# Kernel tuning notes

Measured on AMD Instinct MI355X. Metric: run time of the kernel, lower is better.

Reference implementation:

```python
import jax, jax.numpy as jnp
import numpy as np

D_MODEL = 4096
N_EXPERTS = 64
LN_EPS = 1e-5


def setup_inputs() -> dict:
    key = jax.random.key(0)
    k_x, k_w, k_b = jax.random.split(key, 3)
    x = jax.random.normal(k_x, (4, 4096, D_MODEL), dtype=jnp.float32)
    # LayerNorm affine params (torch defaults: ones / zeros)
    gamma = jnp.ones((D_MODEL,), dtype=jnp.float32)
    beta = jnp.zeros((D_MODEL,), dtype=jnp.float32)
    # Linear(d_model, n): weight (n, d), bias (n) — kaiming-uniform-ish init
    bound = 1.0 / np.sqrt(D_MODEL)
    W = jax.random.uniform(k_w, (N_EXPERTS, D_MODEL), dtype=jnp.float32, minval=-bound, maxval=bound)
    b = jax.random.uniform(k_b, (N_EXPERTS,), dtype=jnp.float32, minval=-bound, maxval=bound)
    return {"x": x, "gamma": gamma, "beta": beta, "W": W, "b": b, "top_k": 2}


def reference(x, gamma, beta, W, b, top_k):
    # LayerNorm over last dim
    mu = jnp.mean(x, axis=-1, keepdims=True)
    var = jnp.mean(jnp.square(x - mu), axis=-1, keepdims=True)
    xn = (x - mu) * jax.lax.rsqrt(var + LN_EPS) * gamma + beta
    # Gate projection: (B,T,d) @ (d,n) -> (B,T,n)
    logits = jnp.einsum('btd,nd->btn', xn, W) + b
    weights = jax.nn.softmax(logits, axis=-1)  # (B,T,n)
    k = min(int(top_k), weights.shape[-1])
    topk_vals, indices = jax.lax.top_k(weights, k)  # (B,T,k)
    # scatter top-k values back to dense (B,T,n), then renormalize
    onehot = jax.nn.one_hot(indices, weights.shape[-1], dtype=weights.dtype)  # (B,T,k,n)
    sparse_w = jnp.einsum('btkn,btk->btn', onehot, topk_vals)
    sparse_w = sparse_w / (jnp.sum(sparse_w, axis=-1, keepdims=True) + 1e-8)
    # load-balance (entropy) loss on dense weights
    mean_w = jnp.mean(weights, axis=(0, 1))  # (n,)
    lb_loss = -jnp.sum(mean_w * jnp.log(mean_w + 1e-8))
    return sparse_w, indices, lb_loss
```

## Files before the change

kernel.cpp:

```cpp
#include <hip/hip_runtime.h>
#include <math.h>

#define D_MODEL 4096
#define N_EXP   64
#define N_ROWS  16384
#define LN_EPS  1e-5f
#define TMB     64
#define NBLK    (N_ROWS / TMB)

typedef __attribute__((ext_vector_type(4))) float f32x4;
typedef __attribute__((ext_vector_type(8))) short s16x8;

struct U4 { unsigned v[4]; };

__device__ __forceinline__ unsigned pkt(float a, float b) {
  unsigned ua = __builtin_bit_cast(unsigned, a);
  unsigned ub = __builtin_bit_cast(unsigned, b);
  return (ua >> 16) | (ub & 0xffff0000u);
}
__device__ __forceinline__ float lo2f(unsigned p) { return __builtin_bit_cast(float, p << 16); }
__device__ __forceinline__ float hi2f(unsigned p) { return __builtin_bit_cast(float, p & 0xffff0000u); }

__device__ __forceinline__ void split8(const float* f, U4& u1, U4& u2, U4& u3) {
#pragma unroll
  for (int i = 0; i < 4; ++i) {
    const float a = f[2 * i], b = f[2 * i + 1];
    const unsigned p1 = pkt(a, b);
    const float ra = a - lo2f(p1), rb = b - hi2f(p1);
    const unsigned p2 = pkt(ra, rb);
    const float sa = ra - lo2f(p2), sb = rb - hi2f(p2);
    u1.v[i] = p1; u2.v[i] = p2; u3.v[i] = pkt(sa, sb);
  }
}


__global__ __launch_bounds__(64) void prep_bpre(
    const float* __restrict__ W, const float* __restrict__ gamma,
    float* __restrict__ Bpre)
{
  const int b = blockIdx.x;
  const int kb32 = b >> 2, j0 = b & 3;
  const int L = threadIdx.x, q = L >> 4, c = L & 15;
  const int n  = j0 * 16 + c;
  const int k0 = kb32 * 32 + q * 8;
  const float4 w0 = *(const float4*)(W + (size_t)n * D_MODEL + k0);
  const float4 w1 = *(const float4*)(W + (size_t)n * D_MODEL + k0 + 4);
  const float4 g0 = *(const float4*)(gamma + k0);
  const float4 g1 = *(const float4*)(gamma + k0 + 4);
  float f[8] = {w0.x * g0.x, w0.y * g0.y, w0.z * g0.z, w0.w * g0.w,
                w1.x * g1.x, w1.y * g1.y, w1.z * g1.z, w1.w * g1.w};
  U4 u1, u2, u3;
  split8(f, u1, u2, u3);
  const size_t base = ((size_t)kb32 * 12 + j0 * 3) * 64 + L;
  *(float4*)(Bpre + (base + 0 * 64) * 4) = __builtin_bit_cast(float4, u1);
  *(float4*)(Bpre + (base + 1 * 64) * 4) = __builtin_bit_cast(float4, u2);
  *(float4*)(Bpre + (base + 2 * 64) * 4) = __builtin_bit_cast(float4, u3);
}

__global__ __launch_bounds__(256) void prep_gc(
    const float* __restrict__ W, const float* __restrict__ gamma,
    const float* __restrict__ beta, const float* __restrict__ bias,
    float* __restrict__ G, float* __restrict__ C)
{
  const int e = blockIdx.x, t = threadIdx.x;
  float sg = 0.f, sb = 0.f;
#pragma unroll
  for (int i = 0; i < 4; ++i) {
    const int d = (i * 256 + t) * 4;
    const float4 wv = *(const float4*)(W + (size_t)e * D_MODEL + d);
    const float4 gv = *(const float4*)(gamma + d);
    const float4 bv = *(const float4*)(beta + d);
    sg += wv.x * gv.x + wv.y * gv.y + wv.z * gv.z + wv.w * gv.w;
    sb += wv.x * bv.x + wv.y * bv.y + wv.z * bv.z + wv.w * bv.w;
  }
#pragma unroll
  for (int o = 32; o > 0; o >>= 1) {
    sg += __shfl_xor(sg, o, 64);
    sb += __shfl_xor(sb, o, 64);
  }
  __shared__ float rg_[4], rb_[4];
  const int wid = t >> 6, ln = t & 63;
  if (ln == 0) { rg_[wid] = sg; rb_[wid] = sb; }
  __syncthreads();
  if (t == 0) {
    G[e] = rg_[0] + rg_[1] + rg_[2] + rg_[3];
    C[e] = rb_[0] + rb_[1] + rb_[2] + rb_[3] + bias[e];
  }
}

__device__ __forceinline__ void loadA64(const float* aptr, int K0, float4 A[4]) {
  const float* ap = aptr + K0;
#pragma unroll
  for (int s = 0; s < 2; ++s) {
    A[2 * s]     = *(const float4*)(ap + s * 32);
    A[2 * s + 1] = *(const float4*)(ap + s * 32 + 4);
  }
}

__device__ __forceinline__ void gload_lds16(const float* g, const float4* l) {
  __builtin_amdgcn_global_load_lds(
      (const __attribute__((address_space(1))) void*)(g),
      (__attribute__((address_space(3))) void*)(l),
      16, 0, 0);
}

__device__ __forceinline__ void stage_chunk64(const float* __restrict__ Bpre,
                                              float4* dstbase, int kb32g, int g, int L)
{
  const float* src = Bpre + (((size_t)kb32g * 12 + g * 6) * 64 + L) * 4;
  float4* dst = dstbase + (size_t)(g * 6) * 64;
#pragma unroll
  for (int i = 0; i < 6; ++i)
    gload_lds16(src + (size_t)i * 256, dst + (size_t)i * 64);
}

__device__ __forceinline__ void compute_chunk64(
    const float4* __restrict__ buf, int L,
    const float4 A[4], f32x4 acc[4], float& Sp, float& Qp)
{
  const int PA[6] = {0, 0, 1, 0, 1, 2};
  const int PB[6] = {0, 1, 0, 2, 1, 0};
#pragma unroll
  for (int s = 0; s < 2; ++s) {
    s16x8 bf[4][3];
#pragma unroll
    for (int j0 = 0; j0 < 4; ++j0)
#pragma unroll
      for (int tt = 0; tt < 3; ++tt)
        bf[j0][tt] = __builtin_bit_cast(s16x8, buf[(size_t)(s * 12 + j0 * 3 + tt) * 64 + L]);
    const float4 a0 = A[2 * s], a1 = A[2 * s + 1];
    const float f[8] = {a0.x, a0.y, a0.z, a0.w, a1.x, a1.y, a1.z, a1.w};
#pragma unroll
    for (int i = 0; i < 8; ++i) { Sp += f[i]; Qp = fmaf(f[i], f[i], Qp); }
    U4 u1, u2, u3;
    split8(f, u1, u2, u3);
    const s16x8 af[3] = {__builtin_bit_cast(s16x8, u1),
                         __builtin_bit_cast(s16x8, u2),
                         __builtin_bit_cast(s16x8, u3)};
#pragma unroll
    for (int p = 0; p < 6; ++p)
#pragma unroll
      for (int j0 = 0; j0 < 4; ++j0)
        acc[j0] = __builtin_amdgcn_mfma_f32_16x16x32_bf16(af[PA[p]], bf[j0][PB[p]],
                                                          acc[j0], 0, 0, 0);
  }
}

__global__ __launch_bounds__(512, 2) void router_main(
    const float* __restrict__ x, const float* __restrict__ Bpre,
    const float* __restrict__ G, const float* __restrict__ C,
    float* __restrict__ out_sw, float* __restrict__ out_idx,
    float* __restrict__ out_partials, int k)
{
  const int t = threadIdx.x, w = t >> 6, L = t & 63;
  const int q = L >> 4, c = L & 15;
  const int g = w & 3;
  const int ks = w >> 2;
  const int blk = blockIdx.x;
  const int row0 = blk * TMB + g * 16;
  const int Kbase = ks * 2048;
  const int kb32base = ks * 64;

  const float* aptr = x + (size_t)(row0 + c) * D_MODEL + q * 8;

  union Smem {
    float4 B[2][2][24 * 64];
    struct { float red[4][64][19]; float sm[4][64]; } ep;
  };
  __shared__ Smem S;

  f32x4 acc[4];
#pragma unroll
  for (int j0 = 0; j0 < 4; ++j0) acc[j0] = (f32x4){0.f, 0.f, 0.f, 0.f};
  float Sp = 0.f, Qp = 0.f;

  float4 A0[4], A1[4];
  loadA64(aptr, Kbase, A0);
  stage_chunk64(Bpre, S.B[ks][0], kb32base, g, L);
  __syncthreads();

  for (int kb = 0; kb < 32; kb += 2) {
    stage_chunk64(Bpre, S.B[ks][1], kb32base + (kb + 1) * 2, g, L);
    loadA64(aptr, Kbase + (kb + 1) * 64, A1);
    compute_chunk64(S.B[ks][0], L, A0, acc, Sp, Qp);
    __syncthreads();

    if (kb + 2 < 32) stage_chunk64(Bpre, S.B[ks][0], kb32base + (kb + 2) * 2, g, L);
    loadA64(aptr, Kbase + ((kb + 2) & 31) * 64, A0);
    compute_chunk64(S.B[ks][1], L, A1, acc, Sp, Qp);
    __syncthreads();
  }

#pragma unroll
  for (int o = 16; o <= 32; o <<= 1) {
    Sp += __shfl_xor(Sp, o, 64);
    Qp += __shfl_xor(Qp, o, 64);
  }

  if (ks == 1) {
    float* dst = &S.ep.red[g][L][0];
#pragma unroll
    for (int j0 = 0; j0 < 4; ++j0)
#pragma unroll
      for (int i = 0; i < 4; ++i) dst[j0 * 4 + i] = acc[j0][i];
    dst[16] = Sp; dst[17] = Qp;
  }
  __syncthreads();

  if (ks == 0) {
    const float* sp_ = &S.ep.red[g][L][0];
#pragma unroll
    for (int j0 = 0; j0 < 4; ++j0)
#pragma unroll
      for (int i = 0; i < 4; ++i) acc[j0][i] += sp_[j0 * 4 + i];
    Sp += sp_[16]; Qp += sp_[17];

    const float mu = Sp * (1.f / D_MODEL);
    const float rs = rsqrtf(Qp * (1.f / D_MODEL) - mu * mu + LN_EPS);

    float Gv[4], Cv[4];
#pragma unroll
    for (int j0 = 0; j0 < 4; ++j0) { Gv[j0] = G[16 * j0 + c]; Cv[j0] = C[16 * j0 + c]; }

    float mw[4] = {0.f, 0.f, 0.f, 0.f};
#pragma unroll
    for (int i = 0; i < 4; ++i) {
      const int rloc = 4 * q + i;
      const int row  = row0 + rloc;
      const float mui = __shfl(mu, rloc, 64);
      const float rsi = __shfl(rs, rloc, 64);
      float l[4];
#pragma unroll
      for (int j0 = 0; j0 < 4; ++j0)
        l[j0] = rsi * (acc[j0][i] - mui * Gv[j0]) + Cv[j0];
      float mx = fmaxf(fmaxf(l[0], l[1]), fmaxf(l[2], l[3]));
#pragma unroll
      for (int o = 1; o < 16; o <<= 1) mx = fmaxf(mx, __shfl_xor(mx, o, 64));
      float p[4], ss = 0.f;
#pragma unroll
      for (int j0 = 0; j0 < 4; ++j0) { p[j0] = __expf(l[j0] - mx); ss += p[j0]; }
#pragma unroll
      for (int o = 1; o < 16; o <<= 1) ss += __shfl_xor(ss, o, 64);
      float wv[4];
#pragma unroll
      for (int j0 = 0; j0 < 4; ++j0) { wv[j0] = p[j0] / ss; mw[j0] += wv[j0]; }

      int ch[4];
      float denom = 0.f;
      for (int kk = 0; kk < k && kk < 4; ++kk) {
        float vb = -1.f; int eb = 1 << 30;
#pragma unroll
        for (int j0 = 0; j0 < 4; ++j0) {
          const int e = 16 * j0 + c;
          bool skip = false;
          for (int z = 0; z < kk; ++z) skip |= (ch[z] == e);
          const float cand = skip ? -1.f : wv[j0];
          if (cand > vb || (cand == vb && e < eb)) { vb = cand; eb = e; }
        }
#pragma unroll
        for (int o = 1; o < 16; o <<= 1) {
          const float ov = __shfl_xor(vb, o, 64);
          const int   oe = __shfl_xor(eb, o, 64);
          if (ov > vb || (ov == vb && oe < eb)) { vb = ov; eb = oe; }
        }
        ch[kk] = eb; denom += vb;
        if (c == 0) out_idx[(size_t)row * k + kk] = (float)eb;
      }
      denom += 1e-8f;
#pragma unroll
      for (int j0 = 0; j0 < 4; ++j0) {
        const int e = 16 * j0 + c;
        bool sel = false;
        for (int z = 0; z < k && z < 4; ++z) sel |= (ch[z] == e);
        out_sw[(size_t)row * N_EXP + e] = sel ? wv[j0] / denom : 0.f;
      }
    }

#pragma unroll
    for (int j0 = 0; j0 < 4; ++j0)
#pragma unroll
      for (int o = 16; o <= 32; o <<= 1) mw[j0] += __shfl_xor(mw[j0], o, 64);
    if (q == 0) {
#pragma unroll
      for (int j0 = 0; j0 < 4; ++j0) S.ep.sm[g][16 * j0 + c] = mw[j0];
    }
  }
  __syncthreads();
  if (t < 64)
    out_partials[blk * 64 + t] = S.ep.sm[0][t] + S.ep.sm[1][t] + S.ep.sm[2][t] + S.ep.sm[3][t];
}

__global__ __launch_bounds__(256) void loss_kernel(
    const float* __restrict__ partials, float* __restrict__ out_loss)
{
  const int t = threadIdx.x, e = t & 63, qq = t >> 6;
  float s = 0.f;
#pragma unroll 8
  for (int b = 0; b < 64; ++b) s += partials[(qq * 64 + b) * 64 + e];
  __shared__ float sh[256];
  sh[t] = s;
  __syncthreads();
  if (t < 64) {
    const float m = (sh[t] + sh[64 + t] + sh[128 + t] + sh[192 + t]) * (1.f / N_ROWS);
    float v = -m * logf(m + 1e-8f);
#pragma unroll
    for (int o = 32; o > 0; o >>= 1) v += __shfl_xor(v, o, 64);
    if (t == 0) out_loss[0] = v;
  }
}

extern "C" void kernel_launch(void* const* d_in, const int* in_sizes, int n_in,
                              void* d_out, int out_size, void* d_ws, size_t ws_size,
                              hipStream_t stream)
{
  const float* x     = (const float*)d_in[0];
  const float* gamma = (const float*)d_in[1];
  const float* beta  = (const float*)d_in[2];
  const float* W     = (const float*)d_in[3];
  const float* bias  = (const float*)d_in[4];

  float* ws       = (float*)d_ws;
  float* Bpre     = ws;
  float* G        = ws + 393216;
  float* C        = ws + 393280;
  float* partials = ws + 393344;

  int k = (out_size - N_ROWS * N_EXP - 1) / N_ROWS;
  if (k < 1) k = 1;
  if (k > 4) k = 4;

  float* out      = (float*)d_out;
  float* out_sw   = out;
  float* out_idx  = out + (size_t)N_ROWS * N_EXP;
  float* out_loss = out + (size_t)N_ROWS * N_EXP + (size_t)N_ROWS * k;

  hipLaunchKernelGGL(prep_bpre, dim3(512), dim3(64), 0, stream, W, gamma, Bpre);
  hipLaunchKernelGGL(prep_gc, dim3(N_EXP), dim3(256), 0, stream, W, gamma, beta, bias, G, C);
  hipLaunchKernelGGL(router_main, dim3(NBLK), dim3(512), 0, stream,
                     x, Bpre, G, C, out_sw, out_idx, partials, k);
  hipLaunchKernelGGL(loss_kernel, dim3(1), dim3(256), 0, stream, partials, out_loss);
}
```

Baseline: 421.4 us.

## Halve row tile to 32 and interleave K halves across warps with shared B buffer

Shrinks each block from 64 rows with 8 waves to 32 rows with 4 waves, doubling the grid to 512 blocks. The two K-split wave pairs now share one staged B chunk per step and take alternating 32-wide K slices, instead of each half of the K range having its own LDS buffer. The aim is better CU occupancy and load balance with a smaller LDS footprint. The cost is that each staged B tile is reused across fewer rows, so B traffic from L2 roughly doubles. The loss reduction is updated for the larger partials array.

```diff
diff --git a/kernel.cpp b/kernel.cpp
--- a/kernel.cpp
+++ b/kernel.cpp
@@ -5,8 +5,9 @@
 #define N_EXP   64
 #define N_ROWS  16384
 #define LN_EPS  1e-5f
-#define TMB     64
+#define TMB     32
 #define NBLK    (N_ROWS / TMB)
+#define NSTEP   64
 
 typedef __attribute__((ext_vector_type(4))) float f32x4;
 typedef __attribute__((ext_vector_type(8))) short s16x8;
@@ -88,15 +89,6 @@
   }
 }
 
-__device__ __forceinline__ void loadA64(const float* aptr, int K0, float4 A[4]) {
-  const float* ap = aptr + K0;
-#pragma unroll
-  for (int s = 0; s < 2; ++s) {
-    A[2 * s]     = *(const float4*)(ap + s * 32);
-    A[2 * s + 1] = *(const float4*)(ap + s * 32 + 4);
-  }
-}
-
 __device__ __forceinline__ void gload_lds16(const float* g, const float4* l) {
   __builtin_amdgcn_global_load_lds(
       (const __attribute__((address_space(1))) void*)(g),
@@ -104,49 +96,52 @@
       16, 0, 0);
 }
 
-__device__ __forceinline__ void stage_chunk64(const float* __restrict__ Bpre,
-                                              float4* dstbase, int kb32g, int g, int L)
-{
-  const float* src = Bpre + (((size_t)kb32g * 12 + g * 6) * 64 + L) * 4;
-  float4* dst = dstbase + (size_t)(g * 6) * 64;
+__device__ __forceinline__ void stage24(const float* __restrict__ Bpre,
+                                        float4* dst, int nk, int w, int L)
+{
+  const float* src = Bpre + (((size_t)nk * 24 + w * 6) * 64 + L) * 4;
+  float4* d = dst + (size_t)(w * 6) * 64;
 #pragma unroll
   for (int i = 0; i < 6; ++i)
-    gload_lds16(src + (size_t)i * 256, dst + (size_t)i * 64);
-}
-
-__device__ __forceinline__ void compute_chunk64(
-    const float4* __restrict__ buf, int L,
-    const float4 A[4], f32x4 acc[4], float& Sp, float& Qp)
+    gload_lds16(src + (size_t)i * 256, d + (size_t)i * 64);
+}
+
+__device__ __forceinline__ void loadA32(const float* aptr, int j, int ks, float4 A[2]) {
+  const float* ap = aptr + (size_t)(j * 2 + ks) * 32;
+  A[0] = *(const float4*)(ap);
+  A[1] = *(const float4*)(ap + 4);
+}
+
+__device__ __forceinline__ void compute_step(
+    const float4* __restrict__ buf, int ks, int L,
+    const float4 A[2], f32x4 acc[4], float& Sp, float& Qp)
 {
   const int PA[6] = {0, 0, 1, 0, 1, 2};
   const int PB[6] = {0, 1, 0, 2, 1, 0};
-#pragma unroll
-  for (int s = 0; s < 2; ++s) {
-    s16x8 bf[4][3];
+  s16x8 bf[4][3];
+#pragma unroll
+  for (int j0 = 0; j0 < 4; ++j0)
+#pragma unroll
+    for (int tt = 0; tt < 3; ++tt)
+      bf[j0][tt] = __builtin_bit_cast(s16x8, buf[(size_t)(ks * 12 + j0 * 3 + tt) * 64 + L]);
+  const float4 a0 = A[0], a1 = A[1];
+  const float f[8] = {a0.x, a0.y, a0.z, a0.w, a1.x, a1.y, a1.z, a1.w};
+#pragma unroll
+  for (int i = 0; i < 8; ++i) { Sp += f[i]; Qp = fmaf(f[i], f[i], Qp); }
+  U4 u1, u2, u3;
+  split8(f, u1, u2, u3);
+  const s16x8 af[3] = {__builtin_bit_cast(s16x8, u1),
+                       __builtin_bit_cast(s16x8, u2),
+                       __builtin_bit_cast(s16x8, u3)};
+#pragma unroll
+  for (int p = 0; p < 6; ++p)
 #pragma unroll
     for (int j0 = 0; j0 < 4; ++j0)
-#pragma unroll
-      for (int tt = 0; tt < 3; ++tt)
-        bf[j0][tt] = __builtin_bit_cast(s16x8, buf[(size_t)(s * 12 + j0 * 3 + tt) * 64 + L]);
-    const float4 a0 = A[2 * s], a1 = A[2 * s + 1];
-    const float f[8] = {a0.x, a0.y, a0.z, a0.w, a1.x, a1.y, a1.z, a1.w};
-#pragma unroll
-    for (int i = 0; i < 8; ++i) { Sp += f[i]; Qp = fmaf(f[i], f[i], Qp); }
-    U4 u1, u2, u3;
-    split8(f, u1, u2, u3);
-    const s16x8 af[3] = {__builtin_bit_cast(s16x8, u1),
-                         __builtin_bit_cast(s16x8, u2),
-                         __builtin_bit_cast(s16x8, u3)};
-#pragma unroll
-    for (int p = 0; p < 6; ++p)
-#pragma unroll
-      for (int j0 = 0; j0 < 4; ++j0)
-        acc[j0] = __builtin_amdgcn_mfma_f32_16x16x32_bf16(af[PA[p]], bf[j0][PB[p]],
-                                                          acc[j0], 0, 0, 0);
-  }
-}
-
-__global__ __launch_bounds__(512, 2) void router_main(
+      acc[j0] = __builtin_amdgcn_mfma_f32_16x16x32_bf16(af[PA[p]], bf[j0][PB[p]],
+                                                        acc[j0], 0, 0, 0);
+}
+
+__global__ __launch_bounds__(256, 2) void router_main(
     const float* __restrict__ x, const float* __restrict__ Bpre,
     const float* __restrict__ G, const float* __restrict__ C,
     float* __restrict__ out_sw, float* __restrict__ out_idx,
@@ -154,18 +149,16 @@
 {
   const int t = threadIdx.x, w = t >> 6, L = t & 63;
   const int q = L >> 4, c = L & 15;
-  const int g = w & 3;
-  const int ks = w >> 2;
+  const int g = w & 1;
+  const int ks = w >> 1;
   const int blk = blockIdx.x;
   const int row0 = blk * TMB + g * 16;
-  const int Kbase = ks * 2048;
-  const int kb32base = ks * 64;
 
   const float* aptr = x + (size_t)(row0 + c) * D_MODEL + q * 8;
 
   union Smem {
-    float4 B[2][2][24 * 64];
-    struct { float red[4][64][19]; float sm[4][64]; } ep;
+    float4 B[2][24 * 64];
+    struct { float red[2][64][19]; float sm[2][64]; } ep;
   };
   __shared__ Smem S;
 
@@ -174,20 +167,20 @@
   for (int j0 = 0; j0 < 4; ++j0) acc[j0] = (f32x4){0.f, 0.f, 0.f, 0.f};
   float Sp = 0.f, Qp = 0.f;
 
-  float4 A0[4], A1[4];
-  loadA64(aptr, Kbase, A0);
-  stage_chunk64(Bpre, S.B[ks][0], kb32base, g, L);
-  __syncthreads();
-
-  for (int kb = 0; kb < 32; kb += 2) {
-    stage_chunk64(Bpre, S.B[ks][1], kb32base + (kb + 1) * 2, g, L);
-    loadA64(aptr, Kbase + (kb + 1) * 64, A1);
-    compute_chunk64(S.B[ks][0], L, A0, acc, Sp, Qp);
+  float4 A0[2], A1[2];
+  loadA32(aptr, 0, ks, A0);
+  stage24(Bpre, S.B[0], 0, w, L);
+  __syncthreads();
+
+  for (int j = 0; j < NSTEP; j += 2) {
+    stage24(Bpre, S.B[1], j + 1, w, L);
+    loadA32(aptr, j + 1, ks, A1);
+    compute_step(S.B[0], ks, L, A0, acc, Sp, Qp);
     __syncthreads();
 
-    if (kb + 2 < 32) stage_chunk64(Bpre, S.B[ks][0], kb32base + (kb + 2) * 2, g, L);
-    loadA64(aptr, Kbase + ((kb + 2) & 31) * 64, A0);
-    compute_chunk64(S.B[ks][1], L, A1, acc, Sp, Qp);
+    if (j + 2 < NSTEP) stage24(Bpre, S.B[0], j + 2, w, L);
+    loadA32(aptr, (j + 2) & (NSTEP - 1), ks, A0);
+    compute_step(S.B[1], ks, L, A1, acc, Sp, Qp);
     __syncthreads();
   }
 
@@ -287,7 +280,7 @@
   }
   __syncthreads();
   if (t < 64)
-    out_partials[blk * 64 + t] = S.ep.sm[0][t] + S.ep.sm[1][t] + S.ep.sm[2][t] + S.ep.sm[3][t];
+    out_partials[blk * 64 + t] = S.ep.sm[0][t] + S.ep.sm[1][t];
 }
 
 __global__ __launch_bounds__(256) void loss_kernel(
@@ -296,7 +289,7 @@
   const int t = threadIdx.x, e = t & 63, qq = t >> 6;
   float s = 0.f;
 #pragma unroll 8
-  for (int b = 0; b < 64; ++b) s += partials[(qq * 64 + b) * 64 + e];
+  for (int b = 0; b < 128; ++b) s += partials[(qq * 128 + b) * 64 + e];
   __shared__ float sh[256];
   sh[t] = s;
   __syncthreads();
@@ -336,7 +329,7 @@
 
   hipLaunchKernelGGL(prep_bpre, dim3(512), dim3(64), 0, stream, W, gamma, Bpre);
   hipLaunchKernelGGL(prep_gc, dim3(N_EXP), dim3(256), 0, stream, W, gamma, beta, bias, G, C);
-  hipLaunchKernelGGL(router_main, dim3(NBLK), dim3(512), 0, stream,
+  hipLaunchKernelGGL(router_main, dim3(NBLK), dim3(256), 0, stream,
                      x, Bpre, G, C, out_sw, out_idx, partials, k);
   hipLaunchKernelGGL(loss_kernel, dim3(1), dim3(256), 0, stream, partials, out_loss);
 }
```

New measurement: 424.0 us. About the same (+0.6%).
